# Performance work log

Hardware: AMD Instinct MI355X
Metric: run time of the kernel (lower is better)

## Reference

```python
import jax, jax.numpy as jnp
import numpy as np

H_MAX = 0.05
TIME_LEN = 5  # t = linspace(0, 1, 5); uniform segments of length 0.25
N_STEPS = int(np.ceil(0.25 / H_MAX))  # Euler steps per segment = 5 (matches torch ode_solve)


def setup_inputs() -> dict:
    key = jax.random.key(0)
    k1, k2, k3, k4, k5 = jax.random.split(key, 5)
    bs, d, hidden = 1024, 1024, 2048
    z0 = jax.random.normal(k1, (bs, d), dtype=jnp.float32)
    t = jnp.linspace(0.0, 1.0, TIME_LEN).astype(jnp.float32)
    # MLP ODEF params: f(z, t) = tanh([z, t] @ W1 + b1) @ W2 + b2
    s1 = 1.0 / np.sqrt(d + 1)
    s2 = 1.0 / np.sqrt(hidden)
    W1 = jax.random.uniform(k2, (d + 1, hidden), jnp.float32, -s1, s1)
    b1 = jax.random.uniform(k3, (hidden,), jnp.float32, -s1, s1)
    W2 = jax.random.uniform(k4, (hidden, d), jnp.float32, -s2, s2)
    b2 = jax.random.uniform(k5, (d,), jnp.float32, -s2, s2)
    return {"z0": z0, "t": t, "W1": W1, "b1": b1, "W2": W2, "b2": b2}


def _f(z, t_scalar, W1, b1, W2, b2):
    # z: [bs, d]; t_scalar broadcast as an extra input feature
    bs = z.shape[0]
    zt = jnp.concatenate([z, jnp.full((bs, 1), t_scalar, dtype=z.dtype)], axis=1)
    h = jnp.tanh(zt @ W1 + b1)
    return h @ W2 + b2


def _ode_solve(z0, t0, t1, W1, b1, W2, b2):
    # Euler: z <- z + h * f(z, t), N_STEPS fixed steps (h_max = 0.05)
    h = (t1 - t0) / N_STEPS

    def step(carry, _):
        z, t = carry
        z = z + h * _f(z, t, W1, b1, W2, b2)
        return (z, t + h), None

    (z, _), _ = jax.lax.scan(step, (z0, t0), None, length=N_STEPS)
    return z


def reference(z0, t, W1, b1, W2, b2):
    # NeuralODE.forward with return_whole_sequence=False: returns z at final time point.
    z = z0
    for i in range(TIME_LEN - 1):  # small fixed loop over time checkpoints
        z = _ode_solve(z, t[i], t[i + 1], W1, b1, W2, b2)
    return z
```

## Files before the change

### kernel.cpp

```cpp
#include <hip/hip_runtime.h>
#include <cstdint>
#include <cstddef>


typedef __bf16 bf16x8 __attribute__((ext_vector_type(8)));
typedef float f32x4 __attribute__((ext_vector_type(4)));

#define WAITV(N) asm volatile("s_waitcnt vmcnt(" #N ") lgkmcnt(0)" ::: "memory")
#define BARRIER() asm volatile("s_barrier" ::: "memory")

__device__ __forceinline__ unsigned short f2bf(float f) {
  union { float f; unsigned u; } v; v.f = f;
  unsigned r = v.u + 0x7fffu + ((v.u >> 16) & 1u);
  return (unsigned short)(r >> 16);
}

__device__ __forceinline__ float fast_tanh(float x) {
  float e = __builtin_amdgcn_exp2f(x * 2.8853900817779268f);
  return 1.0f - 2.0f * __builtin_amdgcn_rcpf(1.0f + e);
}

__global__ void transpose_to_bf16(const float* __restrict__ in,
                                  unsigned short* __restrict__ out,
                                  int rows, int cols) {
  __shared__ float tile[32][33];
  int c0 = blockIdx.x * 32, r0 = blockIdx.y * 32;
  int tx = threadIdx.x, ty = threadIdx.y;
#pragma unroll
  for (int j = 0; j < 32; j += 8)
    tile[ty + j][tx] = in[(size_t)(r0 + ty + j) * cols + (c0 + tx)];
  __syncthreads();
#pragma unroll
  for (int j = 0; j < 32; j += 8)
    out[(size_t)(c0 + ty + j) * rows + (r0 + tx)] = f2bf(tile[tx][ty + j]);
}

__global__ void prep_misc(const float* __restrict__ z0,
                          float* __restrict__ zf,
                          unsigned short* __restrict__ zbf,
                          const float* __restrict__ W1,
                          float* __restrict__ w1l, int n, int nl) {
  int i = blockIdx.x * blockDim.x + threadIdx.x;
  if (i < n) { float v = z0[i]; zf[i] = v; zbf[i] = f2bf(v); }
  if (i < nl) { w1l[i] = W1[(size_t)1024 * 2048 + i]; }
}

__device__ __forceinline__ void stage64(const unsigned short* __restrict__ g,
                                        size_t ld, int row0, int k0,
                                        unsigned short* lds, int tid) {
  int r = tid >> 3;
  int c = (tid & 7) ^ (r & 7);
  __builtin_amdgcn_global_load_lds(
      (const __attribute__((address_space(1))) void*)(
          g + (size_t)(row0 + r) * ld + k0 + c * 8),
      (__attribute__((address_space(3))) void*)(lds + tid * 8), 16, 0, 0);
}

__device__ __forceinline__ bf16x8 frag_ld(const unsigned short* lds, int row,
                                          int chunk_logical, int x) {
  return *(const bf16x8*)(lds + row * 64 + ((chunk_logical ^ x) << 3));
}

__global__ __launch_bounds__(512, 1) void gemm1_kernel(
    const unsigned short* __restrict__ Zb,
    const unsigned short* __restrict__ W1T,
    unsigned short* __restrict__ H,
    const float* __restrict__ b1, const float* __restrict__ w1l, float tval) {
  __shared__ __align__(16) unsigned short lds[24576];
  const int tid = threadIdx.x;
  const int lane = tid & 63, wid = tid >> 6;
  const int l15 = lane & 15, q = lane >> 4, x = l15 & 7;
  const int bid = blockIdx.x;
  const int xcd = bid & 7, loc = bid >> 3;
  const int mt = (loc & 3) | ((xcd & 3) << 2);
  const int nt = (loc >> 2) | ((xcd >> 2) << 3);
  const int m0 = mt * 64, n0 = nt * 128;

  f32x4 acc[2][2] = {};

  auto stage_tile = [&](int t, int b) {
    int k = t * 64;
    unsigned short* p = lds + b * 12288;
    stage64(Zb, 1024, m0, k, p, tid);
    stage64(W1T, 1024, n0, k, p + 4096, tid);
    stage64(W1T, 1024, n0 + 64, k, p + 8192, tid);
  };
  auto compute = [&](int b) {
    const unsigned short* A = lds + b * 12288 + (wid & 1) * 2048;
    const unsigned short* B = lds + b * 12288 + 4096 + (wid >> 1) * 2048;
#pragma unroll
    for (int kk = 0; kk < 2; ++kk) {
      bf16x8 a[2], bb[2];
#pragma unroll
      for (int im = 0; im < 2; ++im)
        a[im] = frag_ld(A, im * 16 + l15, (kk << 2) + q, x);
#pragma unroll
      for (int jn = 0; jn < 2; ++jn)
        bb[jn] = frag_ld(B, jn * 16 + l15, (kk << 2) + q, x);
#pragma unroll
      for (int im = 0; im < 2; ++im)
#pragma unroll
        for (int jn = 0; jn < 2; ++jn)
          acc[im][jn] = __builtin_amdgcn_mfma_f32_16x16x32_bf16(
              a[im], bb[jn], acc[im][jn], 0, 0, 0);
    }
  };

  stage_tile(0, 0);
  stage_tile(1, 1);
  for (int i = 0; i < 15; ++i) {
    WAITV(3);
    BARRIER();
    compute(i & 1);
    if (i < 14) {
      BARRIER();
      stage_tile(i + 2, i & 1);
    }
  }
  WAITV(0);
  BARRIER();
  compute(1);

#pragma unroll
  for (int jn = 0; jn < 2; ++jn) {
    int col = n0 + (wid >> 1) * 32 + jn * 16 + l15;
    float bb = b1[col] + tval * w1l[col];
#pragma unroll
    for (int im = 0; im < 2; ++im) {
      int rowb = m0 + (wid & 1) * 32 + im * 16 + q * 4;
#pragma unroll
      for (int r = 0; r < 4; ++r)
        H[(size_t)(rowb + r) * 2048 + col] =
            f2bf(fast_tanh(acc[im][jn][r] + bb));
    }
  }
}

__global__ __launch_bounds__(512, 1) void gemm2_kernel(
    const unsigned short* __restrict__ Hb,
    const unsigned short* __restrict__ W2T,
    const float* __restrict__ b2,
    const float* __restrict__ zf,
    float* __restrict__ outf,
    unsigned short* __restrict__ zbf,
    float h) {
  __shared__ __align__(16) unsigned short lds[32768];
  const int tid = threadIdx.x;
  const int lane = tid & 63, wid = tid >> 6;
  const int l15 = lane & 15, q = lane >> 4, x = l15 & 7;
  const int kh = wid >> 2, mh = (wid >> 1) & 1, nh = wid & 1;
  const int bid = blockIdx.x;
  const int xcd = bid & 7, loc = bid >> 3;
  const int mt = (loc & 3) | ((xcd & 3) << 2);
  const int nt = (loc >> 2) | ((xcd >> 2) << 3);
  const int m0 = mt * 64, n0 = nt * 64;

  f32x4 acc[2][2] = {};

  auto stage_tile = [&](int t, int b) {
    int k = t * 64;
    unsigned short* p = lds + b * 16384;
    stage64(Hb, 2048, m0, k, p, tid);
    stage64(Hb, 2048, m0, k + 1024, p + 4096, tid);
    stage64(W2T, 2048, n0, k, p + 8192, tid);
    stage64(W2T, 2048, n0, k + 1024, p + 12288, tid);
  };
  auto compute = [&](int b) {
    const unsigned short* A = lds + b * 16384 + kh * 4096 + mh * 2048;
    const unsigned short* B = lds + b * 16384 + 8192 + kh * 4096 + nh * 2048;
#pragma unroll
    for (int kk = 0; kk < 2; ++kk) {
      bf16x8 a[2], bb[2];
#pragma unroll
      for (int im = 0; im < 2; ++im)
        a[im] = frag_ld(A, im * 16 + l15, (kk << 2) + q, x);
#pragma unroll
      for (int jn = 0; jn < 2; ++jn)
        bb[jn] = frag_ld(B, jn * 16 + l15, (kk << 2) + q, x);
#pragma unroll
      for (int im = 0; im < 2; ++im)
#pragma unroll
        for (int jn = 0; jn < 2; ++jn)
          acc[im][jn] = __builtin_amdgcn_mfma_f32_16x16x32_bf16(
              a[im], bb[jn], acc[im][jn], 0, 0, 0);
    }
  };

  stage_tile(0, 0);
  stage_tile(1, 1);
  for (int i = 0; i < 15; ++i) {
    WAITV(4);
    BARRIER();
    compute(i & 1);
    if (i < 14) {
      BARRIER();
      stage_tile(i + 2, i & 1);
    }
  }
  WAITV(0);
  BARRIER();
  compute(1);

  __syncthreads();
  float* red = (float*)lds;
  const int region = (mh * 2 + nh) * 1056;
  if (kh == 1) {
#pragma unroll
    for (int im = 0; im < 2; ++im)
#pragma unroll
      for (int jn = 0; jn < 2; ++jn) {
        int c = jn * 16 + l15;
#pragma unroll
        for (int r = 0; r < 4; ++r)
          red[region + (im * 16 + q * 4 + r) * 33 + c] = acc[im][jn][r];
      }
  }
  __syncthreads();
  if (kh == 0) {
#pragma unroll
    for (int jn = 0; jn < 2; ++jn) {
      int coll = nh * 32 + jn * 16 + l15;
      int col = n0 + coll;
      float bb = b2[col];
#pragma unroll
      for (int im = 0; im < 2; ++im) {
        int rowl = im * 16 + q * 4;
#pragma unroll
        for (int r = 0; r < 4; ++r) {
          float s = acc[im][jn][r] +
                    red[region + (rowl + r) * 33 + jn * 16 + l15];
          size_t gidx = (size_t)(m0 + mh * 32 + rowl + r) * 1024 + col;
          float zv = zf[gidx] + h * (s + bb);
          outf[gidx] = zv;
          zbf[gidx] = f2bf(zv);
        }
      }
    }
  }
}

extern "C" void kernel_launch(void* const* d_in, const int* in_sizes, int n_in,
                              void* d_out, int out_size, void* d_ws,
                              size_t ws_size, hipStream_t stream) {
  const float* z0 = (const float*)d_in[0];
  const float* W1 = (const float*)d_in[2];
  const float* b1 = (const float*)d_in[3];
  const float* W2 = (const float*)d_in[4];
  const float* b2 = (const float*)d_in[5];
  float* out = (float*)d_out;

  char* ws = (char*)d_ws;
  unsigned short* W1T = (unsigned short*)(ws + 0);
  unsigned short* W2T = (unsigned short*)(ws + (4u << 20));
  unsigned short* zbf = (unsigned short*)(ws + (8u << 20));
  unsigned short* Hbf = (unsigned short*)(ws + (10u << 20));
  float* zf = (float*)(ws + (14u << 20));
  float* w1l = (float*)(ws + (18u << 20));

  transpose_to_bf16<<<dim3(64, 32), dim3(32, 8), 0, stream>>>(W1, W1T, 1024, 2048);
  transpose_to_bf16<<<dim3(32, 64), dim3(32, 8), 0, stream>>>(W2, W2T, 2048, 1024);
  prep_misc<<<4096, 256, 0, stream>>>(z0, zf, zbf, W1, w1l, 1024 * 1024, 2048);

  const float h = 0.05f;
  for (int seg = 0; seg < 4; ++seg) {
    float tcur = 0.25f * (float)seg;
    for (int j = 0; j < 5; ++j) {
      gemm1_kernel<<<256, 512, 0, stream>>>(zbf, W1T, Hbf, b1, w1l, tcur);
      bool last = (seg == 3 && j == 4);
      float* outf = last ? out : zf;
      gemm2_kernel<<<256, 512, 0, stream>>>(Hbf, W2T, b2, zf, outf, zbf, h);
      tcur += h;
    }
  }
}
```

Baseline: 450.8 us.

## Load A fragments directly to registers and triple-buffer B tiles with one barrier

Both GEMM kernels now read their A operand (activations) straight from global memory into registers, double-buffered in register sets one tile ahead, instead of staging it through LDS. Only the B weights go through LDS, now in a three-buffer rotation with a single barrier per K-step instead of two, and the main loop is fully unrolled. The aim is to cut LDS traffic and barrier stalls and to overlap loads with MFMA work. In exchange, A is read with uncoalesced 16-byte per-lane loads, and register pressure from the extra fragment sets goes up.

```diff
diff --git a/kernel.cpp b/kernel.cpp
--- a/kernel.cpp
+++ b/kernel.cpp
@@ -8,6 +8,8 @@
 
 #define WAITV(N) asm volatile("s_waitcnt vmcnt(" #N ") lgkmcnt(0)" ::: "memory")
 #define BARRIER() asm volatile("s_barrier" ::: "memory")
+#define SEP() asm volatile("" ::: "memory")
+#define MFMA(a, b, c) __builtin_amdgcn_mfma_f32_16x16x32_bf16(a, b, c, 0, 0, 0)
 
 __device__ __forceinline__ unsigned short f2bf(float f) {
   union { float f; unsigned u; } v; v.f = f;
@@ -47,18 +49,18 @@
 
 __device__ __forceinline__ void stage64(const unsigned short* __restrict__ g,
                                         size_t ld, int row0, int k0,
-                                        unsigned short* lds, int tid) {
+                                        unsigned short* lp, int tid) {
   int r = tid >> 3;
   int c = (tid & 7) ^ (r & 7);
   __builtin_amdgcn_global_load_lds(
       (const __attribute__((address_space(1))) void*)(
           g + (size_t)(row0 + r) * ld + k0 + c * 8),
-      (__attribute__((address_space(3))) void*)(lds + tid * 8), 16, 0, 0);
-}
-
-__device__ __forceinline__ bf16x8 frag_ld(const unsigned short* lds, int row,
+      (__attribute__((address_space(3))) void*)(lp + tid * 8), 16, 0, 0);
+}
+
+__device__ __forceinline__ bf16x8 frag_ld(const unsigned short* lp, int row,
                                           int chunk_logical, int x) {
-  return *(const bf16x8*)(lds + row * 64 + ((chunk_logical ^ x) << 3));
+  return *(const bf16x8*)(lp + row * 64 + ((chunk_logical ^ x) << 3));
 }
 
 __global__ __launch_bounds__(512, 1) void gemm1_kernel(
@@ -76,62 +78,96 @@
   const int nt = (loc >> 2) | ((xcd >> 2) << 3);
   const int m0 = mt * 64, n0 = nt * 128;
 
-  f32x4 acc[2][2] = {};
-
-  auto stage_tile = [&](int t, int b) {
+  unsigned short* const buf0 = lds;
+  unsigned short* const buf1 = lds + 8192;
+  unsigned short* const buf2 = lds + 16384;
+
+  f32x4 acc00 = {}, acc01 = {}, acc10 = {}, acc11 = {};
+  bf16x8 a0A, a1A, a2A, a3A, a0B, a1B, a2B, a3B;
+
+  const unsigned short* const Abase =
+      Zb + (size_t)(m0 + (wid & 1) * 32 + l15) * 1024 + q * 8;
+
+  auto stage_tile = [&](int t, unsigned short* p) {
     int k = t * 64;
-    unsigned short* p = lds + b * 12288;
-    stage64(Zb, 1024, m0, k, p, tid);
-    stage64(W1T, 1024, n0, k, p + 4096, tid);
-    stage64(W1T, 1024, n0 + 64, k, p + 8192, tid);
+    stage64(W1T, 1024, n0, k, p, tid);
+    stage64(W1T, 1024, n0 + 64, k, p + 4096, tid);
   };
-  auto compute = [&](int b) {
-    const unsigned short* A = lds + b * 12288 + (wid & 1) * 2048;
-    const unsigned short* B = lds + b * 12288 + 4096 + (wid >> 1) * 2048;
-#pragma unroll
-    for (int kk = 0; kk < 2; ++kk) {
-      bf16x8 a[2], bb[2];
-#pragma unroll
-      for (int im = 0; im < 2; ++im)
-        a[im] = frag_ld(A, im * 16 + l15, (kk << 2) + q, x);
-#pragma unroll
-      for (int jn = 0; jn < 2; ++jn)
-        bb[jn] = frag_ld(B, jn * 16 + l15, (kk << 2) + q, x);
-#pragma unroll
-      for (int im = 0; im < 2; ++im)
-#pragma unroll
-        for (int jn = 0; jn < 2; ++jn)
-          acc[im][jn] = __builtin_amdgcn_mfma_f32_16x16x32_bf16(
-              a[im], bb[jn], acc[im][jn], 0, 0, 0);
-    }
-  };
-
-  stage_tile(0, 0);
-  stage_tile(1, 1);
-  for (int i = 0; i < 15; ++i) {
-    WAITV(3);
-    BARRIER();
-    compute(i & 1);
-    if (i < 14) {
-      BARRIER();
-      stage_tile(i + 2, i & 1);
-    }
-  }
+
+#define LOADA(t, s)                                         \
+  do {                                                      \
+    const unsigned short* _p = Abase + (t) * 64;            \
+    a0##s = *(const bf16x8*)(_p);                           \
+    a1##s = *(const bf16x8*)(_p + 32);                      \
+    a2##s = *(const bf16x8*)(_p + 16 * 1024);               \
+    a3##s = *(const bf16x8*)(_p + 16 * 1024 + 32);          \
+  } while (0)
+
+#define COMPUTE(p, s)                                       \
+  do {                                                      \
+    const unsigned short* _B = (p) + (wid >> 1) * 2048;     \
+    bf16x8 _b0 = frag_ld(_B, l15, q, x);                    \
+    bf16x8 _b1 = frag_ld(_B, 16 + l15, q, x);               \
+    bf16x8 _b2 = frag_ld(_B, l15, 4 + q, x);                \
+    bf16x8 _b3 = frag_ld(_B, 16 + l15, 4 + q, x);           \
+    acc00 = MFMA(a0##s, _b0, acc00);                        \
+    acc01 = MFMA(a0##s, _b1, acc01);                        \
+    acc10 = MFMA(a2##s, _b0, acc10);                        \
+    acc11 = MFMA(a2##s, _b1, acc11);                        \
+    acc00 = MFMA(a1##s, _b2, acc00);                        \
+    acc01 = MFMA(a1##s, _b3, acc01);                        \
+    acc10 = MFMA(a3##s, _b2, acc10);                        \
+    acc11 = MFMA(a3##s, _b3, acc11);                        \
+  } while (0)
+
+#define STEP(t, sc, sn, pc, pn, W) \
+  LOADA((t) + 1, sn);              \
+  WAITV(W);                        \
+  BARRIER();                       \
+  stage_tile((t) + 2, pn);         \
+  COMPUTE(pc, sc)
+
+  LOADA(0, A);
+  stage_tile(0, buf0);
+  SEP();
+  stage_tile(1, buf1);
+
+  STEP(0, A, B, buf0, buf2, 0);
+  STEP(1, B, A, buf1, buf0, 6);
+  STEP(2, A, B, buf2, buf1, 6);
+  STEP(3, B, A, buf0, buf2, 6);
+  STEP(4, A, B, buf1, buf0, 6);
+  STEP(5, B, A, buf2, buf1, 6);
+  STEP(6, A, B, buf0, buf2, 6);
+  STEP(7, B, A, buf1, buf0, 6);
+  STEP(8, A, B, buf2, buf1, 6);
+  STEP(9, B, A, buf0, buf2, 6);
+  STEP(10, A, B, buf1, buf0, 6);
+  STEP(11, B, A, buf2, buf1, 6);
+  STEP(12, A, B, buf0, buf2, 6);
+  STEP(13, B, A, buf1, buf0, 6);
+  LOADA(15, B);
+  WAITV(6);
+  BARRIER();
+  COMPUTE(buf2, A);
   WAITV(0);
   BARRIER();
-  compute(1);
-
-#pragma unroll
-  for (int jn = 0; jn < 2; ++jn) {
-    int col = n0 + (wid >> 1) * 32 + jn * 16 + l15;
-    float bb = b1[col] + tval * w1l[col];
-#pragma unroll
-    for (int im = 0; im < 2; ++im) {
-      int rowb = m0 + (wid & 1) * 32 + im * 16 + q * 4;
-#pragma unroll
-      for (int r = 0; r < 4; ++r)
-        H[(size_t)(rowb + r) * 2048 + col] =
-            f2bf(fast_tanh(acc[im][jn][r] + bb));
+  COMPUTE(buf0, B);
+#undef LOADA
+#undef COMPUTE
+#undef STEP
+
+  {
+    const int colb = n0 + (wid >> 1) * 32 + l15;
+    const int rowb = m0 + (wid & 1) * 32 + q * 4;
+    const float bia0 = b1[colb] + tval * w1l[colb];
+    const float bia1 = b1[colb + 16] + tval * w1l[colb + 16];
+#pragma unroll
+    for (int r = 0; r < 4; ++r) {
+      H[(size_t)(rowb + r) * 2048 + colb]        = f2bf(fast_tanh(acc00[r] + bia0));
+      H[(size_t)(rowb + r) * 2048 + colb + 16]   = f2bf(fast_tanh(acc01[r] + bia1));
+      H[(size_t)(rowb + 16 + r) * 2048 + colb]      = f2bf(fast_tanh(acc10[r] + bia0));
+      H[(size_t)(rowb + 16 + r) * 2048 + colb + 16] = f2bf(fast_tanh(acc11[r] + bia1));
     }
   }
 }
@@ -144,7 +180,7 @@
     float* __restrict__ outf,
     unsigned short* __restrict__ zbf,
     float h) {
-  __shared__ __align__(16) unsigned short lds[32768];
+  __shared__ __align__(16) unsigned short lds[24576];
   const int tid = threadIdx.x;
   const int lane = tid & 63, wid = tid >> 6;
   const int l15 = lane & 15, q = lane >> 4, x = l15 & 7;
@@ -155,86 +191,123 @@
   const int nt = (loc >> 2) | ((xcd >> 2) << 3);
   const int m0 = mt * 64, n0 = nt * 64;
 
-  f32x4 acc[2][2] = {};
-
-  auto stage_tile = [&](int t, int b) {
+  unsigned short* const buf0 = lds;
+  unsigned short* const buf1 = lds + 8192;
+  unsigned short* const buf2 = lds + 16384;
+
+  f32x4 acc00 = {}, acc01 = {}, acc10 = {}, acc11 = {};
+  bf16x8 a0A, a1A, a2A, a3A, a0B, a1B, a2B, a3B;
+
+  const unsigned short* const Abase =
+      Hb + (size_t)(m0 + mh * 32 + l15) * 2048 + kh * 1024 + q * 8;
+
+  auto stage_tile = [&](int t, unsigned short* p) {
     int k = t * 64;
-    unsigned short* p = lds + b * 16384;
-    stage64(Hb, 2048, m0, k, p, tid);
-    stage64(Hb, 2048, m0, k + 1024, p + 4096, tid);
-    stage64(W2T, 2048, n0, k, p + 8192, tid);
-    stage64(W2T, 2048, n0, k + 1024, p + 12288, tid);
+    stage64(W2T, 2048, n0, k, p, tid);
+    stage64(W2T, 2048, n0, k + 1024, p + 4096, tid);
   };
-  auto compute = [&](int b) {
-    const unsigned short* A = lds + b * 16384 + kh * 4096 + mh * 2048;
-    const unsigned short* B = lds + b * 16384 + 8192 + kh * 4096 + nh * 2048;
-#pragma unroll
-    for (int kk = 0; kk < 2; ++kk) {
-      bf16x8 a[2], bb[2];
-#pragma unroll
-      for (int im = 0; im < 2; ++im)
-        a[im] = frag_ld(A, im * 16 + l15, (kk << 2) + q, x);
-#pragma unroll
-      for (int jn = 0; jn < 2; ++jn)
-        bb[jn] = frag_ld(B, jn * 16 + l15, (kk << 2) + q, x);
-#pragma unroll
-      for (int im = 0; im < 2; ++im)
-#pragma unroll
-        for (int jn = 0; jn < 2; ++jn)
-          acc[im][jn] = __builtin_amdgcn_mfma_f32_16x16x32_bf16(
-              a[im], bb[jn], acc[im][jn], 0, 0, 0);
-    }
-  };
-
-  stage_tile(0, 0);
-  stage_tile(1, 1);
-  for (int i = 0; i < 15; ++i) {
-    WAITV(4);
-    BARRIER();
-    compute(i & 1);
-    if (i < 14) {
-      BARRIER();
-      stage_tile(i + 2, i & 1);
-    }
-  }
+
+#define LOADA(t, s)                                         \
+  do {                                                      \
+    const unsigned short* _p = Abase + (t) * 64;            \
+    a0##s = *(const bf16x8*)(_p);                           \
+    a1##s = *(const bf16x8*)(_p + 32);                      \
+    a2##s = *(const bf16x8*)(_p + 16 * 2048);               \
+    a3##s = *(const bf16x8*)(_p + 16 * 2048 + 32);          \
+  } while (0)
+
+#define COMPUTE(p, s)                                       \
+  do {                                                      \
+    const unsigned short* _B = (p) + kh * 4096 + nh * 2048; \
+    bf16x8 _b0 = frag_ld(_B, l15, q, x);                    \
+    bf16x8 _b1 = frag_ld(_B, 16 + l15, q, x);               \
+    bf16x8 _b2 = frag_ld(_B, l15, 4 + q, x);                \
+    bf16x8 _b3 = frag_ld(_B, 16 + l15, 4 + q, x);           \
+    acc00 = MFMA(a0##s, _b0, acc00);                        \
+    acc01 = MFMA(a0##s, _b1, acc01);                        \
+    acc10 = MFMA(a2##s, _b0, acc10);                        \
+    acc11 = MFMA(a2##s, _b1, acc11);                        \
+    acc00 = MFMA(a1##s, _b2, acc00);                        \
+    acc01 = MFMA(a1##s, _b3, acc01);                        \
+    acc10 = MFMA(a3##s, _b2, acc10);                        \
+    acc11 = MFMA(a3##s, _b3, acc11);                        \
+  } while (0)
+
+#define STEP(t, sc, sn, pc, pn, W) \
+  LOADA((t) + 1, sn);              \
+  WAITV(W);                        \
+  BARRIER();                       \
+  stage_tile((t) + 2, pn);         \
+  COMPUTE(pc, sc)
+
+  LOADA(0, A);
+  stage_tile(0, buf0);
+  SEP();
+  stage_tile(1, buf1);
+
+  STEP(0, A, B, buf0, buf2, 0);
+  STEP(1, B, A, buf1, buf0, 6);
+  STEP(2, A, B, buf2, buf1, 6);
+  STEP(3, B, A, buf0, buf2, 6);
+  STEP(4, A, B, buf1, buf0, 6);
+  STEP(5, B, A, buf2, buf1, 6);
+  STEP(6, A, B, buf0, buf2, 6);
+  STEP(7, B, A, buf1, buf0, 6);
+  STEP(8, A, B, buf2, buf1, 6);
+  STEP(9, B, A, buf0, buf2, 6);
+  STEP(10, A, B, buf1, buf0, 6);
+  STEP(11, B, A, buf2, buf1, 6);
+  STEP(12, A, B, buf0, buf2, 6);
+  STEP(13, B, A, buf1, buf0, 6);
+  LOADA(15, B);
+  WAITV(6);
+  BARRIER();
+  COMPUTE(buf2, A);
   WAITV(0);
   BARRIER();
-  compute(1);
+  COMPUTE(buf0, B);
+#undef LOADA
+#undef COMPUTE
+#undef STEP
 
   __syncthreads();
   float* red = (float*)lds;
   const int region = (mh * 2 + nh) * 1056;
+  const int rl = q * 4;
   if (kh == 1) {
 #pragma unroll
-    for (int im = 0; im < 2; ++im)
-#pragma unroll
-      for (int jn = 0; jn < 2; ++jn) {
-        int c = jn * 16 + l15;
-#pragma unroll
-        for (int r = 0; r < 4; ++r)
-          red[region + (im * 16 + q * 4 + r) * 33 + c] = acc[im][jn][r];
-      }
+    for (int r = 0; r < 4; ++r) {
+      red[region + (rl + r) * 33 + l15]           = acc00[r];
+      red[region + (rl + r) * 33 + 16 + l15]      = acc01[r];
+      red[region + (16 + rl + r) * 33 + l15]      = acc10[r];
+      red[region + (16 + rl + r) * 33 + 16 + l15] = acc11[r];
+    }
   }
   __syncthreads();
   if (kh == 0) {
-#pragma unroll
-    for (int jn = 0; jn < 2; ++jn) {
-      int coll = nh * 32 + jn * 16 + l15;
-      int col = n0 + coll;
-      float bb = b2[col];
-#pragma unroll
-      for (int im = 0; im < 2; ++im) {
-        int rowl = im * 16 + q * 4;
-#pragma unroll
-        for (int r = 0; r < 4; ++r) {
-          float s = acc[im][jn][r] +
-                    red[region + (rowl + r) * 33 + jn * 16 + l15];
-          size_t gidx = (size_t)(m0 + mh * 32 + rowl + r) * 1024 + col;
-          float zv = zf[gidx] + h * (s + bb);
-          outf[gidx] = zv;
-          zbf[gidx] = f2bf(zv);
-        }
-      }
+    const int colb = n0 + nh * 32 + l15;
+    const float bb0 = b2[colb], bb1 = b2[colb + 16];
+#pragma unroll
+    for (int r = 0; r < 4; ++r) {
+      float s00 = acc00[r] + red[region + (rl + r) * 33 + l15];
+      size_t g00 = (size_t)(m0 + mh * 32 + rl + r) * 1024 + colb;
+      float z00 = zf[g00] + h * (s00 + bb0);
+      outf[g00] = z00; zbf[g00] = f2bf(z00);
+
+      float s01 = acc01[r] + red[region + (rl + r) * 33 + 16 + l15];
+      size_t g01 = g00 + 16;
+      float z01 = zf[g01] + h * (s01 + bb1);
+      outf[g01] = z01; zbf[g01] = f2bf(z01);
+
+      float s10 = acc10[r] + red[region + (16 + rl + r) * 33 + l15];
+      size_t g10 = (size_t)(m0 + mh * 32 + 16 + rl + r) * 1024 + colb;
+      float z10 = zf[g10] + h * (s10 + bb0);
+      outf[g10] = z10; zbf[g10] = f2bf(z10);
+
+      float s11 = acc11[r] + red[region + (16 + rl + r) * 33 + 16 + l15];
+      size_t g11 = g10 + 16;
+      float z11 = zf[g11] + h * (s11 + bb1);
+      outf[g11] = z11; zbf[g11] = f2bf(z11);
     }
   }
 }
```

Result: slower. 906.0 us (+101.0%).

## Triple-buffer LDS staging in both GEMMs to drop per-iteration second barrier

Applied to the files above, without the earlier changes.

Both GEMM kernels move from a double-buffered to a triple-buffered LDS pipeline, and the K loop is fully unrolled with explicit buffer rotation. The load for tile t+2 is now issued right after the barrier and before computing tile t. This removes the second barrier each iteration and gives the async global-to-LDS loads more time to land behind the MFMA work. The cost is 1.5x the LDS footprint per block (72KB and 96KB) and larger unrolled code.

```diff
diff --git a/kernel.cpp b/kernel.cpp
--- a/kernel.cpp
+++ b/kernel.cpp
@@ -8,6 +8,7 @@
 
 #define WAITV(N) asm volatile("s_waitcnt vmcnt(" #N ") lgkmcnt(0)" ::: "memory")
 #define BARRIER() asm volatile("s_barrier" ::: "memory")
+#define SEP() asm volatile("" ::: "memory")
 
 __device__ __forceinline__ unsigned short f2bf(float f) {
   union { float f; unsigned u; } v; v.f = f;
@@ -47,18 +48,18 @@
 
 __device__ __forceinline__ void stage64(const unsigned short* __restrict__ g,
                                         size_t ld, int row0, int k0,
-                                        unsigned short* lds, int tid) {
+                                        unsigned short* lp, int tid) {
   int r = tid >> 3;
   int c = (tid & 7) ^ (r & 7);
   __builtin_amdgcn_global_load_lds(
       (const __attribute__((address_space(1))) void*)(
           g + (size_t)(row0 + r) * ld + k0 + c * 8),
-      (__attribute__((address_space(3))) void*)(lds + tid * 8), 16, 0, 0);
-}
-
-__device__ __forceinline__ bf16x8 frag_ld(const unsigned short* lds, int row,
+      (__attribute__((address_space(3))) void*)(lp + tid * 8), 16, 0, 0);
+}
+
+__device__ __forceinline__ bf16x8 frag_ld(const unsigned short* lp, int row,
                                           int chunk_logical, int x) {
-  return *(const bf16x8*)(lds + row * 64 + ((chunk_logical ^ x) << 3));
+  return *(const bf16x8*)(lp + row * 64 + ((chunk_logical ^ x) << 3));
 }
 
 __global__ __launch_bounds__(512, 1) void gemm1_kernel(
@@ -66,7 +67,7 @@
     const unsigned short* __restrict__ W1T,
     unsigned short* __restrict__ H,
     const float* __restrict__ b1, const float* __restrict__ w1l, float tval) {
-  __shared__ __align__(16) unsigned short lds[24576];
+  __shared__ __align__(16) unsigned short lds[36864];
   const int tid = threadIdx.x;
   const int lane = tid & 63, wid = tid >> 6;
   const int l15 = lane & 15, q = lane >> 4, x = l15 & 7;
@@ -76,18 +77,21 @@
   const int nt = (loc >> 2) | ((xcd >> 2) << 3);
   const int m0 = mt * 64, n0 = nt * 128;
 
+  unsigned short* const buf0 = lds;
+  unsigned short* const buf1 = lds + 12288;
+  unsigned short* const buf2 = lds + 24576;
+
   f32x4 acc[2][2] = {};
 
-  auto stage_tile = [&](int t, int b) {
+  auto stage_tile = [&](int t, unsigned short* p) {
     int k = t * 64;
-    unsigned short* p = lds + b * 12288;
     stage64(Zb, 1024, m0, k, p, tid);
     stage64(W1T, 1024, n0, k, p + 4096, tid);
     stage64(W1T, 1024, n0 + 64, k, p + 8192, tid);
   };
-  auto compute = [&](int b) {
-    const unsigned short* A = lds + b * 12288 + (wid & 1) * 2048;
-    const unsigned short* B = lds + b * 12288 + 4096 + (wid >> 1) * 2048;
+  auto compute = [&](const unsigned short* p) {
+    const unsigned short* A = p + (wid & 1) * 2048;
+    const unsigned short* B = p + 4096 + (wid >> 1) * 2048;
 #pragma unroll
     for (int kk = 0; kk < 2; ++kk) {
       bf16x8 a[2], bb[2];
@@ -106,20 +110,37 @@
     }
   };
 
-  stage_tile(0, 0);
-  stage_tile(1, 1);
-  for (int i = 0; i < 15; ++i) {
-    WAITV(3);
-    BARRIER();
-    compute(i & 1);
-    if (i < 14) {
-      BARRIER();
-      stage_tile(i + 2, i & 1);
-    }
-  }
+#define STEP(t, pc, pn) \
+  WAITV(3);             \
+  BARRIER();            \
+  stage_tile((t) + 2, pn); \
+  compute(pc)
+
+  stage_tile(0, buf0);
+  SEP();
+  stage_tile(1, buf1);
+
+  STEP(0, buf0, buf2);
+  STEP(1, buf1, buf0);
+  STEP(2, buf2, buf1);
+  STEP(3, buf0, buf2);
+  STEP(4, buf1, buf0);
+  STEP(5, buf2, buf1);
+  STEP(6, buf0, buf2);
+  STEP(7, buf1, buf0);
+  STEP(8, buf2, buf1);
+  STEP(9, buf0, buf2);
+  STEP(10, buf1, buf0);
+  STEP(11, buf2, buf1);
+  STEP(12, buf0, buf2);
+  STEP(13, buf1, buf0);
+  WAITV(3);
+  BARRIER();
+  compute(buf2);
   WAITV(0);
   BARRIER();
-  compute(1);
+  compute(buf0);
+#undef STEP
 
 #pragma unroll
   for (int jn = 0; jn < 2; ++jn) {
@@ -144,7 +165,7 @@
     float* __restrict__ outf,
     unsigned short* __restrict__ zbf,
     float h) {
-  __shared__ __align__(16) unsigned short lds[32768];
+  __shared__ __align__(16) unsigned short lds[49152];
   const int tid = threadIdx.x;
   const int lane = tid & 63, wid = tid >> 6;
   const int l15 = lane & 15, q = lane >> 4, x = l15 & 7;
@@ -155,19 +176,22 @@
   const int nt = (loc >> 2) | ((xcd >> 2) << 3);
   const int m0 = mt * 64, n0 = nt * 64;
 
+  unsigned short* const buf0 = lds;
+  unsigned short* const buf1 = lds + 16384;
+  unsigned short* const buf2 = lds + 32768;
+
   f32x4 acc[2][2] = {};
 
-  auto stage_tile = [&](int t, int b) {
+  auto stage_tile = [&](int t, unsigned short* p) {
     int k = t * 64;
-    unsigned short* p = lds + b * 16384;
     stage64(Hb, 2048, m0, k, p, tid);
     stage64(Hb, 2048, m0, k + 1024, p + 4096, tid);
     stage64(W2T, 2048, n0, k, p + 8192, tid);
     stage64(W2T, 2048, n0, k + 1024, p + 12288, tid);
   };
-  auto compute = [&](int b) {
-    const unsigned short* A = lds + b * 16384 + kh * 4096 + mh * 2048;
-    const unsigned short* B = lds + b * 16384 + 8192 + kh * 4096 + nh * 2048;
+  auto compute = [&](const unsigned short* p) {
+    const unsigned short* A = p + kh * 4096 + mh * 2048;
+    const unsigned short* B = p + 8192 + kh * 4096 + nh * 2048;
 #pragma unroll
     for (int kk = 0; kk < 2; ++kk) {
       bf16x8 a[2], bb[2];
@@ -186,20 +210,37 @@
     }
   };
 
-  stage_tile(0, 0);
-  stage_tile(1, 1);
-  for (int i = 0; i < 15; ++i) {
-    WAITV(4);
-    BARRIER();
-    compute(i & 1);
-    if (i < 14) {
-      BARRIER();
-      stage_tile(i + 2, i & 1);
-    }
-  }
+#define STEP(t, pc, pn) \
+  WAITV(4);             \
+  BARRIER();            \
+  stage_tile((t) + 2, pn); \
+  compute(pc)
+
+  stage_tile(0, buf0);
+  SEP();
+  stage_tile(1, buf1);
+
+  STEP(0, buf0, buf2);
+  STEP(1, buf1, buf0);
+  STEP(2, buf2, buf1);
+  STEP(3, buf0, buf2);
+  STEP(4, buf1, buf0);
+  STEP(5, buf2, buf1);
+  STEP(6, buf0, buf2);
+  STEP(7, buf1, buf0);
+  STEP(8, buf2, buf1);
+  STEP(9, buf0, buf2);
+  STEP(10, buf1, buf0);
+  STEP(11, buf2, buf1);
+  STEP(12, buf0, buf2);
+  STEP(13, buf1, buf0);
+  WAITV(4);
+  BARRIER();
+  compute(buf2);
   WAITV(0);
   BARRIER();
-  compute(1);
+  compute(buf0);
+#undef STEP
 
   __syncthreads();
   float* red = (float*)lds;
```

After: 432.3 us. 4.1% less time.
